# Performance work log

Hardware: AMD Instinct MI355X
Metric: run time of the kernel (lower is better)

The kernel has to match this reference:

```python
import jax, jax.numpy as jnp
import numpy as np
from jax import lax

BS, L, HID = 16, 512, 768
H, HD, NREG = 12, 64, 8
R2 = 2 * NREG


def setup_inputs() -> dict:
    key = jax.random.key(0)
    ks = jax.random.split(key, 7)
    s = 1.0 / np.sqrt(HID)
    return {
        "hidden_states": jax.random.normal(ks[0], (BS, L, HID), jnp.float32),
        "K1_w": jax.random.normal(ks[1], (H * HD, HID), jnp.float32) * s,
        "K1_b": jnp.zeros((H * HD,), jnp.float32),
        "V1_w": jax.random.normal(ks[2], (H * HD, HID), jnp.float32) * s,
        "V1_b": jnp.zeros((H * HD,), jnp.float32),
        "reading_head": jax.random.normal(ks[3], (H, HD), jnp.float32) * (1.0 / np.sqrt(HD)),
        "bidirection_weight": jnp.ones((1, 1, H, 1, R2), jnp.float32) * (1.0 / R2),
    }


def _softmax_dim1(x):
    # torch: softmax over length dim (1) plus 1/exp(max) residual term
    m = jnp.max(x, axis=1, keepdims=True)
    e = jnp.exp(x - m)
    return e / jnp.sum(e, axis=1, keepdims=True) + jnp.exp(-m)


def _cummax_idx(e):
    # torch.cummax indices over axis=1 for a bool tensor (ties -> latest index):
    # last True index so far; if no True yet, current index.
    ar = jnp.arange(e.shape[1], dtype=jnp.int32)[None, :, None]
    lt = lax.cummax(jnp.where(e, ar, jnp.int32(-1)), axis=1)
    return jnp.where(lt >= 0, lt, ar)


def reference(hidden_states, K1_w, K1_b, V1_w, V1_b, reading_head, bidirection_weight):
    bs, length, _ = hidden_states.shape
    K1 = jax.nn.relu(hidden_states @ K1_w.T + K1_b).reshape(bs, length, H, HD)
    V1 = jax.nn.relu(hidden_states @ V1_w.T + V1_b).reshape(bs, length, H, HD)

    scores = jnp.einsum("blhn,hn->blh", K1, reading_head)
    events = _softmax_dim1(scores) > (1.5 / length)  # (bs, L, H) bool; fwd==bwd for IC1

    col0 = _cummax_idx(events)  # (bs, L, H)
    rolled = jnp.roll(events, -1, axis=1)
    col1 = jnp.flip(512 - _cummax_idx(jnp.flip(rolled, axis=1)), axis=1)
    col1 = col1.at[:, 0].set(0)

    # sequential shift-register scan over length
    e_seq = jnp.moveaxis(events, 1, 0)  # (L, bs, H)
    f_seq = jnp.moveaxis(col0, 1, 0)
    b_seq = jnp.moveaxis(col1, 1, 0)
    row0 = jnp.concatenate(
        [f_seq[0][:, None], b_seq[0][:, None], jnp.zeros((bs, R2, H), jnp.int32)], axis=1
    )  # (bs, R2+2, H)

    def step(row, inp):
        e, f, b = inp
        reg = jnp.where(e[:, None, :], row[:, :-2], row[:, 2:])  # shift-in on event
        new_row = jnp.concatenate([f[:, None], b[:, None], reg], axis=1)
        return new_row, reg

    _, regs = lax.scan(step, row0, (e_seq[1:], f_seq[1:], b_seq[1:]))
    regs = jnp.concatenate([jnp.zeros((1, bs, R2, H), jnp.int32), regs], axis=0)  # (L,bs,R2,H)
    idx = jnp.moveaxis(regs, 0, 1).reshape(bs, length * R2, H)
    idx = jnp.clip(idx, 0, length - 1)

    V2 = jnp.take_along_axis(V1, idx[..., None], axis=1).reshape(bs, length, R2, H, HD)
    w = bidirection_weight.reshape(H, R2)
    return jnp.einsum("blrhd,hr->blhd", V2, w)  # (bs, L, H, HD)
```

## Files before the change

### kernel.cpp

```cpp
#include <hip/hip_runtime.h>
#include <cstdint>
#include <cstddef>

#define BSZ 16
#define LQ  512
#define HIDDIM 768
#define NH  12
#define HD  64
#define R2V 16
#define NTOT 1536
#define MTOT 8192

typedef __bf16 bf16x8 __attribute__((ext_vector_type(8)));
typedef float  f32x4  __attribute__((ext_vector_type(4)));

__device__ inline unsigned short f2bf(float x) {
    union { float f; unsigned u; } c; c.f = x;
    unsigned r = c.u + 0x7fffu + ((c.u >> 16) & 1u);
    return (unsigned short)(r >> 16);
}

#define NHS4 1572864
#define NW1  147456
#define NW4  294912

__global__ __launch_bounds__(256) void cast_pack(
    const float* __restrict__ hs,
    const float* __restrict__ Kw, const float* __restrict__ Vw,
    const float* __restrict__ Kb, const float* __restrict__ Vb,
    unsigned short* __restrict__ hsb, unsigned short* __restrict__ Wb,
    float* __restrict__ biasp)
{
    const int i = blockIdx.x * 256 + threadIdx.x;
    float4 v; unsigned short* dst;
    if (i < NHS4) {
        v = ((const float4*)hs)[i];
        dst = hsb + (size_t)i * 4;
    } else {
        const int j = i - NHS4;
        v = (j < NW1) ? ((const float4*)Kw)[j] : ((const float4*)Vw)[j - NW1];
        dst = Wb + (size_t)j * 4;
    }
    ushort4 o;
    o.x = f2bf(v.x); o.y = f2bf(v.y); o.z = f2bf(v.z); o.w = f2bf(v.w);
    *(ushort4*)dst = o;
    if (i < 768) { biasp[i] = Kb[i]; biasp[768 + i] = Vb[i]; }
}

#define TBM 128
#define TBN 128
#define TBK 32

#define GLD16(g, l) __builtin_amdgcn_global_load_lds( \
    (const __attribute__((address_space(1))) void*)(g), \
    (__attribute__((address_space(3))) void*)(l), 16, 0, 0)

__global__ __launch_bounds__(256) void gemm_mfma(
    const unsigned short* __restrict__ Abf,
    const unsigned short* __restrict__ Wbf,
    const float* __restrict__ biasp,
    float* __restrict__ K1, float* __restrict__ V1)
{
    __shared__ unsigned short As[TBM * TBK];
    __shared__ unsigned short Bs[TBN * TBK];

    const int n0   = blockIdx.x * TBN;
    const int m0   = blockIdx.y * TBM;
    const int tid  = threadIdx.x;
    const int wid  = tid >> 6;
    const int lane = tid & 63;
    const int wm   = (wid & 1) * 64;
    const int wn   = (wid >> 1) * 64;

    f32x4 acc[4][4] = {};

    const int r0 = wid * 32;
    const int rA = r0 + (lane >> 2);
    const int kp = (lane & 3) * 8;

    const unsigned short* Ap0 = Abf + (size_t)(m0 + rA) * HIDDIM + kp;
    const unsigned short* Ap1 = Abf + (size_t)(m0 + rA + 16) * HIDDIM + kp;
    const unsigned short* Bp0 = Wbf + (size_t)(n0 + rA) * HIDDIM + kp;
    const unsigned short* Bp1 = Wbf + (size_t)(n0 + rA + 16) * HIDDIM + kp;

    unsigned short* AsD0 = &As[r0 * TBK];
    unsigned short* AsD1 = &As[(r0 + 16) * TBK];
    unsigned short* BsD0 = &Bs[r0 * TBK];
    unsigned short* BsD1 = &Bs[(r0 + 16) * TBK];

    const int fm = lane & 15;
    const int fk = (lane >> 4) * 8;

    for (int k0 = 0; k0 < HIDDIM; k0 += TBK) {
        __syncthreads();
        GLD16(Ap0 + k0, AsD0);
        GLD16(Ap1 + k0, AsD1);
        GLD16(Bp0 + k0, BsD0);
        GLD16(Bp1 + k0, BsD1);
        __syncthreads();

        bf16x8 af[4], bfr[4];
        #pragma unroll
        for (int mi = 0; mi < 4; ++mi)
            af[mi] = *reinterpret_cast<const bf16x8*>(&As[(wm + mi * 16 + fm) * TBK + fk]);
        #pragma unroll
        for (int ni = 0; ni < 4; ++ni)
            bfr[ni] = *reinterpret_cast<const bf16x8*>(&Bs[(wn + ni * 16 + fm) * TBK + fk]);
        #pragma unroll
        for (int mi = 0; mi < 4; ++mi)
            #pragma unroll
            for (int ni = 0; ni < 4; ++ni)
                acc[mi][ni] = __builtin_amdgcn_mfma_f32_16x16x32_bf16(
                    af[mi], bfr[ni], acc[mi][ni], 0, 0, 0);
    }

    const bool isK = (n0 < HIDDIM);
    float* __restrict__ dst = isK ? K1 : V1;
    const int nsub = isK ? 0 : HIDDIM;

    #pragma unroll
    for (int ni = 0; ni < 4; ++ni) {
        const int ng = n0 + wn + ni * 16 + (lane & 15);
        const float bv = biasp[ng];
        const int col = ng - nsub;
        #pragma unroll
        for (int mi = 0; mi < 4; ++mi) {
            const int mb = m0 + wm + mi * 16 + (lane >> 4) * 4;
            #pragma unroll
            for (int r = 0; r < 4; ++r)
                dst[(size_t)(mb + r) * HIDDIM + col] = fmaxf(acc[mi][ni][r] + bv, 0.f);
        }
    }
}

#define SINF (1 << 30)

__global__ __launch_bounds__(512) void scores_scan(
    const float* __restrict__ K1,
    const float* __restrict__ rh,
    int* __restrict__ idxbuf)
{
    const int bh   = blockIdx.x;
    const int b    = bh / NH;
    const int h    = bh % NH;
    const int l    = threadIdx.x;
    const int lane = l & 63;
    const int wid  = l >> 6;

    __shared__ float wredA[8];
    __shared__ float wredB[8];
    __shared__ int   wp0[8];
    __shared__ int   wp1[8];
    __shared__ int   wp2[8];
    __shared__ int   ev[LQ];
    __shared__ int   col0[LQ];
    __shared__ int   col1[LQ];
    __shared__ int   E[LQ];

    const float* krow = K1 + ((size_t)(b * LQ + l)) * HIDDIM + h * HD;
    const float* rrow = rh + h * HD;
    float s = 0.f;
    #pragma unroll
    for (int d = 0; d < HD; d += 4) {
        float4 kv = *(const float4*)(krow + d);
        float4 rv = *(const float4*)(rrow + d);
        s += kv.x * rv.x + kv.y * rv.y + kv.z * rv.z + kv.w * rv.w;
    }

    float mx = s;
    #pragma unroll
    for (int off = 32; off > 0; off >>= 1) mx = fmaxf(mx, __shfl_xor(mx, off));
    if (lane == 0) wredA[wid] = mx;
    __syncthreads();
    float m = wredA[0];
    #pragma unroll
    for (int i = 1; i < 8; ++i) m = fmaxf(m, wredA[i]);

    const float e = expf(s - m);
    float sm = e;
    #pragma unroll
    for (int off = 32; off > 0; off >>= 1) sm += __shfl_xor(sm, off);
    if (lane == 0) wredB[wid] = sm;
    __syncthreads();
    float ssum = 0.f;
    #pragma unroll
    for (int i = 0; i < 8; ++i) ssum += wredB[i];

    const float p = e / ssum + expf(-m);
    const int event = (p > (1.5f / 512.0f)) ? 1 : 0;
    ev[l] = event;

    int v = event ? l : -1;
    #pragma unroll
    for (int off = 1; off < 64; off <<= 1) {
        int u = __shfl_up(v, off);
        if (lane >= off) v = (u > v) ? u : v;
    }
    if (lane == 63) wp0[wid] = v;
    __syncthreads();
    int pfx = -1;
    for (int i = 0; i < wid; ++i) pfx = (wp0[i] > pfx) ? wp0[i] : pfx;
    v = (pfx > v) ? pfx : v;
    col0[l] = (v >= 0) ? v : l;

    int v1 = ev[(l + 1) & (LQ - 1)] ? l : SINF;
    #pragma unroll
    for (int off = 1; off < 64; off <<= 1) {
        int u = __shfl_down(v1, off);
        if (lane < 64 - off) v1 = (u < v1) ? u : v1;
    }
    if (lane == 0) wp1[wid] = v1;
    __syncthreads();
    int sfx = SINF;
    for (int i = wid + 1; i < 8; ++i) sfx = (wp1[i] < sfx) ? wp1[i] : sfx;
    v1 = (sfx < v1) ? sfx : v1;
    col1[l] = (l == 0) ? 0 : (((v1 < SINF) ? v1 : l) + 1);

    int c = (l >= 1) ? event : 0;
    #pragma unroll
    for (int off = 1; off < 64; off <<= 1) {
        int u = __shfl_up(c, off);
        if (lane >= off) c += u;
    }
    if (lane == 63) wp2[wid] = c;
    __syncthreads();
    for (int i = 0; i < wid; ++i) c += wp2[i];

    if (l >= 1 && event) E[c - 1] = l;
    __syncthreads();

    int* op = idxbuf + ((size_t)(b * LQ + l) * NH + h) * R2V;
    #pragma unroll
    for (int j = 0; j < 8; ++j) {
        const int k = c - 1 - j;
        int f = 0, bb = 0;
        if (k >= 0) {
            const int t = E[k];
            f  = col0[t - 1];
            bb = col1[t - 1];
        }
        f  = min(max(f, 0), LQ - 1);
        bb = min(max(bb, 0), LQ - 1);
        op[2 * j]     = f;
        op[2 * j + 1] = bb;
    }
}

__global__ __launch_bounds__(256) void gather_out(
    const float* __restrict__ V1,
    const int* __restrict__ idxbuf,
    const float* __restrict__ w,
    float* __restrict__ out)
{
    const int g   = blockIdx.x * 16 + (threadIdx.x >> 4);
    const int t16 = threadIdx.x & 15;
    const int h   = g % NH;
    const int bl  = g / NH;
    const int b   = bl / LQ;

    const int*   ip = idxbuf + (size_t)g * R2V;
    const float* wp = w + h * R2V;

    const int   myidx = ip[t16];
    const float myw   = wp[t16];

    const float* base = V1 + (size_t)b * LQ * HIDDIM + h * HD + t16 * 4;

    float4 acc = make_float4(0.f, 0.f, 0.f, 0.f);
    #pragma unroll
    for (int r = 0; r < R2V; ++r) {
        const int   idx = __shfl(myidx, r, 16);
        const float wr  = __shfl(myw,   r, 16);
        float4 v = *(const float4*)(base + (size_t)idx * HIDDIM);
        acc.x += wr * v.x; acc.y += wr * v.y;
        acc.z += wr * v.z; acc.w += wr * v.w;
    }
    *(float4*)(out + (size_t)g * HD + t16 * 4) = acc;
}

extern "C" void kernel_launch(void* const* d_in, const int* in_sizes, int n_in,
                              void* d_out, int out_size, void* d_ws, size_t ws_size,
                              hipStream_t stream)
{
    (void)in_sizes; (void)n_in; (void)out_size; (void)ws_size;

    const float* hs = (const float*)d_in[0];
    const float* Kw = (const float*)d_in[1];
    const float* Kb = (const float*)d_in[2];
    const float* Vw = (const float*)d_in[3];
    const float* Vb = (const float*)d_in[4];
    const float* rh = (const float*)d_in[5];
    const float* bw = (const float*)d_in[6];
    float* out = (float*)d_out;

    char* ws = (char*)d_ws;
    float*          K1    = (float*)(ws);
    float*          V1    = (float*)(ws + 25165824);
    int*            idxb  = (int*)  (ws + 50331648);
    unsigned short* hsb   = (unsigned short*)(ws + 56623104);
    unsigned short* Wb    = (unsigned short*)(ws + 69206016);
    float*          biasp = (float*)(ws + 71565312);

    cast_pack<<<(NHS4 + NW4) / 256, 256, 0, stream>>>(hs, Kw, Vw, Kb, Vb, hsb, Wb, biasp);

    dim3 g1(NTOT / TBN, MTOT / TBM);
    gemm_mfma<<<g1, 256, 0, stream>>>(hsb, Wb, biasp, K1, V1);

    scores_scan<<<BSZ * NH, LQ, 0, stream>>>(K1, rh, idxb);

    gather_out<<<(BSZ * LQ * NH) / 16, 256, 0, stream>>>(V1, idxb, bw, out);
}
```

Before: 169.0 us.

## Store K1/V1 as bf16 and fuse scan with gather into one kernel

The GEMM epilogue now writes K1 and V1 as bf16, with MFMA operands swapped so each lane holds four consecutive columns and can store them as one vector. This halves the intermediate write and read traffic. The scores/scan kernel is merged with the gather kernel: indices stay in padded shared memory instead of a global idx buffer, and each block gathers bf16 V1 rows to produce its (b,h) outputs. The cost is bf16 rounding of K1, which could flip event thresholds, and of V1, plus a gather that now runs on only 192 blocks and so has less parallelism.

```diff
diff --git a/kernel.cpp b/kernel.cpp
--- a/kernel.cpp
+++ b/kernel.cpp
@@ -19,6 +19,8 @@
     unsigned r = c.u + 0x7fffu + ((c.u >> 16) & 1u);
     return (unsigned short)(r >> 16);
 }
+__device__ inline float bfl(unsigned u) { return __uint_as_float(u << 16); }
+__device__ inline float bfh(unsigned u) { return __uint_as_float(u & 0xffff0000u); }
 
 #define NHS4 1572864
 #define NW1  147456
@@ -59,7 +61,7 @@
     const unsigned short* __restrict__ Abf,
     const unsigned short* __restrict__ Wbf,
     const float* __restrict__ biasp,
-    float* __restrict__ K1, float* __restrict__ V1)
+    unsigned short* __restrict__ K1b, unsigned short* __restrict__ V1b)
 {
     __shared__ unsigned short As[TBM * TBK];
     __shared__ unsigned short Bs[TBN * TBK];
@@ -111,34 +113,42 @@
             #pragma unroll
             for (int ni = 0; ni < 4; ++ni)
                 acc[mi][ni] = __builtin_amdgcn_mfma_f32_16x16x32_bf16(
-                    af[mi], bfr[ni], acc[mi][ni], 0, 0, 0);
+                    bfr[ni], af[mi], acc[mi][ni], 0, 0, 0);
     }
 
     const bool isK = (n0 < HIDDIM);
-    float* __restrict__ dst = isK ? K1 : V1;
+    unsigned short* __restrict__ dst = isK ? K1b : V1b;
     const int nsub = isK ? 0 : HIDDIM;
-
-    #pragma unroll
-    for (int ni = 0; ni < 4; ++ni) {
-        const int ng = n0 + wn + ni * 16 + (lane & 15);
-        const float bv = biasp[ng];
-        const int col = ng - nsub;
-        #pragma unroll
-        for (int mi = 0; mi < 4; ++mi) {
-            const int mb = m0 + wm + mi * 16 + (lane >> 4) * 4;
-            #pragma unroll
-            for (int r = 0; r < 4; ++r)
-                dst[(size_t)(mb + r) * HIDDIM + col] = fmaxf(acc[mi][ni][r] + bv, 0.f);
+    const int mloc = lane & 15;
+    const int nq   = (lane >> 4) * 4;
+
+    #pragma unroll
+    for (int mi = 0; mi < 4; ++mi) {
+        const int mg = m0 + wm + mi * 16 + mloc;
+        #pragma unroll
+        for (int ni = 0; ni < 4; ++ni) {
+            const int ng = n0 + wn + ni * 16 + nq;
+            float4 bv = *(const float4*)(biasp + ng);
+            f32x4 a = acc[mi][ni];
+            ushort4 o;
+            o.x = f2bf(fmaxf(a[0] + bv.x, 0.f));
+            o.y = f2bf(fmaxf(a[1] + bv.y, 0.f));
+            o.z = f2bf(fmaxf(a[2] + bv.z, 0.f));
+            o.w = f2bf(fmaxf(a[3] + bv.w, 0.f));
+            *(ushort4*)(dst + (size_t)mg * HIDDIM + (ng - nsub)) = o;
         }
     }
 }
 
 #define SINF (1 << 30)
-
-__global__ __launch_bounds__(512) void scores_scan(
-    const float* __restrict__ K1,
+#define IXP 17
+
+__global__ __launch_bounds__(512) void scan_gather(
+    const unsigned short* __restrict__ K1b,
+    const unsigned short* __restrict__ V1b,
     const float* __restrict__ rh,
-    int* __restrict__ idxbuf)
+    const float* __restrict__ bw,
+    float* __restrict__ out)
 {
     const int bh   = blockIdx.x;
     const int b    = bh / NH;
@@ -156,15 +166,23 @@
     __shared__ int   col0[LQ];
     __shared__ int   col1[LQ];
     __shared__ int   E[LQ];
-
-    const float* krow = K1 + ((size_t)(b * LQ + l)) * HIDDIM + h * HD;
+    __shared__ int   idxs[LQ * IXP];
+    __shared__ float wsm[R2V];
+
+    if (l < R2V) wsm[l] = bw[h * R2V + l];
+
+    const unsigned short* krow = K1b + ((size_t)(b * LQ + l)) * HIDDIM + h * HD;
     const float* rrow = rh + h * HD;
     float s = 0.f;
     #pragma unroll
-    for (int d = 0; d < HD; d += 4) {
-        float4 kv = *(const float4*)(krow + d);
-        float4 rv = *(const float4*)(rrow + d);
-        s += kv.x * rv.x + kv.y * rv.y + kv.z * rv.z + kv.w * rv.w;
+    for (int c8 = 0; c8 < 8; ++c8) {
+        uint4 kv = *(const uint4*)(krow + c8 * 8);
+        float4 ra = *(const float4*)(rrow + c8 * 8);
+        float4 rb = *(const float4*)(rrow + c8 * 8 + 4);
+        s += bfl(kv.x) * ra.x + bfh(kv.x) * ra.y
+           + bfl(kv.y) * ra.z + bfh(kv.y) * ra.w
+           + bfl(kv.z) * rb.x + bfh(kv.z) * rb.y
+           + bfl(kv.w) * rb.z + bfh(kv.w) * rb.w;
     }
 
     float mx = s;
@@ -229,7 +247,7 @@
     if (l >= 1 && event) E[c - 1] = l;
     __syncthreads();
 
-    int* op = idxbuf + ((size_t)(b * LQ + l) * NH + h) * R2V;
+    int* op = &idxs[l * IXP];
     #pragma unroll
     for (int j = 0; j < 8; ++j) {
         const int k = c - 1 - j;
@@ -239,43 +257,33 @@
             f  = col0[t - 1];
             bb = col1[t - 1];
         }
-        f  = min(max(f, 0), LQ - 1);
-        bb = min(max(bb, 0), LQ - 1);
-        op[2 * j]     = f;
-        op[2 * j + 1] = bb;
-    }
-}
-
-__global__ __launch_bounds__(256) void gather_out(
-    const float* __restrict__ V1,
-    const int* __restrict__ idxbuf,
-    const float* __restrict__ w,
-    float* __restrict__ out)
-{
-    const int g   = blockIdx.x * 16 + (threadIdx.x >> 4);
-    const int t16 = threadIdx.x & 15;
-    const int h   = g % NH;
-    const int bl  = g / NH;
-    const int b   = bl / LQ;
-
-    const int*   ip = idxbuf + (size_t)g * R2V;
-    const float* wp = w + h * R2V;
-
-    const int   myidx = ip[t16];
-    const float myw   = wp[t16];
-
-    const float* base = V1 + (size_t)b * LQ * HIDDIM + h * HD + t16 * 4;
-
-    float4 acc = make_float4(0.f, 0.f, 0.f, 0.f);
-    #pragma unroll
-    for (int r = 0; r < R2V; ++r) {
-        const int   idx = __shfl(myidx, r, 16);
-        const float wr  = __shfl(myw,   r, 16);
-        float4 v = *(const float4*)(base + (size_t)idx * HIDDIM);
-        acc.x += wr * v.x; acc.y += wr * v.y;
-        acc.z += wr * v.z; acc.w += wr * v.w;
-    }
-    *(float4*)(out + (size_t)g * HD + t16 * 4) = acc;
+        op[2 * j]     = min(max(f, 0), LQ - 1);
+        op[2 * j + 1] = min(max(bb, 0), LQ - 1);
+    }
+    __syncthreads();
+
+    const int dsl = lane & 7;
+    const size_t vbase = (size_t)b * LQ * HIDDIM + h * HD + dsl * 8;
+
+    for (int round = 0; round < 8; ++round) {
+        const int lg = round * 64 + wid * 8 + (lane >> 3);
+        const int* ip = &idxs[lg * IXP];
+        float a0 = 0.f, a1 = 0.f, a2 = 0.f, a3 = 0.f;
+        float a4 = 0.f, a5 = 0.f, a6 = 0.f, a7 = 0.f;
+        #pragma unroll
+        for (int r = 0; r < R2V; ++r) {
+            const int row = ip[r];
+            const float wr = wsm[r];
+            uint4 vv = *(const uint4*)(V1b + vbase + (size_t)row * HIDDIM);
+            a0 += wr * bfl(vv.x); a1 += wr * bfh(vv.x);
+            a2 += wr * bfl(vv.y); a3 += wr * bfh(vv.y);
+            a4 += wr * bfl(vv.z); a5 += wr * bfh(vv.z);
+            a6 += wr * bfl(vv.w); a7 += wr * bfh(vv.w);
+        }
+        float* po = out + ((size_t)(b * LQ + lg) * NH + h) * HD + dsl * 8;
+        *(float4*)po       = make_float4(a0, a1, a2, a3);
+        *((float4*)po + 1) = make_float4(a4, a5, a6, a7);
+    }
 }
 
 extern "C" void kernel_launch(void* const* d_in, const int* in_sizes, int n_in,
@@ -294,19 +302,16 @@
     float* out = (float*)d_out;
 
     char* ws = (char*)d_ws;
-    float*          K1    = (float*)(ws);
-    float*          V1    = (float*)(ws + 25165824);
-    int*            idxb  = (int*)  (ws + 50331648);
-    unsigned short* hsb   = (unsigned short*)(ws + 56623104);
-    unsigned short* Wb    = (unsigned short*)(ws + 69206016);
-    float*          biasp = (float*)(ws + 71565312);
+    unsigned short* K1b   = (unsigned short*)(ws);
+    unsigned short* V1b   = (unsigned short*)(ws + 12582912);
+    unsigned short* hsb   = (unsigned short*)(ws + 25165824);
+    unsigned short* Wb    = (unsigned short*)(ws + 37748736);
+    float*          biasp = (float*)(ws + 40108032);
 
     cast_pack<<<(NHS4 + NW4) / 256, 256, 0, stream>>>(hs, Kw, Vw, Kb, Vb, hsb, Wb, biasp);
 
     dim3 g1(NTOT / TBN, MTOT / TBM);
-    gemm_mfma<<<g1, 256, 0, stream>>>(hsb, Wb, biasp, K1, V1);
-
-    scores_scan<<<BSZ * NH, LQ, 0, stream>>>(K1, rh, idxb);
-
-    gather_out<<<(BSZ * LQ * NH) / 16, 256, 0, stream>>>(V1, idxb, bw, out);
-}
+    gemm_mfma<<<g1, 256, 0, stream>>>(hsb, Wb, biasp, K1b, V1b);
+
+    scan_gather<<<BSZ * NH, LQ, 0, stream>>>(K1b, V1b, rh, bw, out);
+}
```

Result: faster. 147.3 us (-12.9%).
